# Optimization experiments

Hardware: AMD Instinct MI355X
Metric: run time of the kernel (lower is better)

## Reference

```python
import jax, jax.numpy as jnp
import numpy as np

NQ = 9  # 9 qubits per 3x3 patch; state shape (M, 2,...,2), axis (NQ-q) holds qubit q (qiskit little-endian)

def _ax(q):
    return NQ - q

def _bcast(theta):
    theta = jnp.asarray(theta)
    if theta.ndim == 1:  # per-patch angle -> broadcast over 8 remaining qubit axes
        return theta.reshape((-1,) + (1,) * (NQ - 1))
    return theta

def apply_1q(state, q, m00, m01, m10, m11):
    ax = _ax(q)
    s0 = jnp.take(state, 0, axis=ax)
    s1 = jnp.take(state, 1, axis=ax)
    return jnp.stack([m00 * s0 + m01 * s1, m10 * s0 + m11 * s1], axis=ax)

def apply_ry(state, q, theta):
    th = _bcast(theta) * 0.5
    c = jnp.cos(th).astype(state.dtype)
    s = jnp.sin(th).astype(state.dtype)
    return apply_1q(state, q, c, -s, s, c)

def apply_rz(state, q, theta):
    th = _bcast(theta) * 0.5
    e = jnp.exp(-1j * th.astype(jnp.complex64))
    return apply_1q(state, q, e, 0.0, 0.0, jnp.conj(e))

def apply_cx(state, c, t):
    axc, axt = _ax(c), _ax(t)
    sc0 = jnp.take(state, 0, axis=axc)
    sc1 = jnp.take(state, 1, axis=axc)
    axt2 = axt - 1 if axt > axc else axt
    sc1 = jnp.flip(sc1, axis=axt2)  # X on target within control=1 subspace
    return jnp.stack([sc0, sc1], axis=axc)

def apply_crx(state, c, t, theta):
    axc, axt = _ax(c), _ax(t)
    sc0 = jnp.take(state, 0, axis=axc)
    sc1 = jnp.take(state, 1, axis=axc)
    axt2 = axt - 1 if axt > axc else axt
    t0 = jnp.take(sc1, 0, axis=axt2)
    t1 = jnp.take(sc1, 1, axis=axt2)
    co = jnp.cos(theta * 0.5)
    si = jnp.sin(theta * 0.5)
    sc1 = jnp.stack([co * t0 - 1j * si * t1, -1j * si * t0 + co * t1], axis=axt2)
    return jnp.stack([sc0, sc1], axis=axc)

def qcnn_batched(angles, w):
    """angles: (M, 9) input rotation angles. w: (42,) shared weights. Returns (M, 3) = [<X>,<Y>,<Z>] on qubit 0."""
    M = angles.shape[0]
    state = jnp.zeros((M,) + (2,) * NQ, dtype=jnp.complex64)
    state = state.at[(slice(None),) + (0,) * NQ].set(1.0)
    for q in range(NQ):  # input encoding
        state = apply_ry(state, q, angles[:, q])
    wi = 0
    # conv1: RY + RZ on all 9 qubits, ring CNOT
    for q in range(NQ):
        state = apply_ry(state, q, w[wi]); wi += 1
    for q in range(NQ):
        state = apply_rz(state, q, w[wi]); wi += 1
    for i in range(NQ):
        state = apply_cx(state, i, (i + 1) % NQ)
    # pool1: 6 CRX gates
    for (c, t) in [(1, 0), (2, 0), (4, 3), (5, 3), (7, 6), (8, 6)]:
        state = apply_crx(state, c, t, w[wi]); wi += 1
    # conv2 on qubits [0,3,6]
    for q in [0, 3, 6]:
        state = apply_ry(state, q, w[wi]); wi += 1
    for q in [0, 3, 6]:
        state = apply_rz(state, q, w[wi]); wi += 1
    for (c, t) in [(0, 3), (3, 6), (6, 0)]:
        state = apply_cx(state, c, t)
    state = apply_ry(state, 0, w[wi])
    state = apply_rz(state, 3, w[wi + 1]); wi += 2
    # pool2
    state = apply_crx(state, 3, 0, w[wi])
    state = apply_crx(state, 3, 6, w[wi + 1])
    state = apply_ry(state, 0, w[wi + 2])
    state = apply_ry(state, 6, w[wi + 3]); wi += 4
    # conv3
    state = apply_ry(state, 0, w[wi])
    state = apply_ry(state, 6, w[wi + 1])
    state = apply_cx(state, 0, 6)
    state = apply_rz(state, 0, w[wi + 2])
    state = apply_rz(state, 6, w[wi + 3]); wi += 4
    # pool3
    state = apply_crx(state, 6, 0, w[wi])
    state = apply_ry(state, 0, w[wi + 1]); wi += 2
    assert wi == 42
    # expectations <X>,<Y>,<Z> on qubit 0 (last axis)
    a0 = jnp.take(state, 0, axis=NQ)
    a1 = jnp.take(state, 1, axis=NQ)
    axes = tuple(range(1, NQ))
    z = jnp.sum(jnp.conj(a0) * a1, axis=axes)
    ex = 2.0 * jnp.real(z)
    ey = 2.0 * jnp.imag(z)
    ez = jnp.sum(jnp.abs(a0) ** 2 - jnp.abs(a1) ** 2, axis=axes)
    return jnp.stack([ex, ey, ez], axis=-1).astype(jnp.float32)

def setup_inputs() -> dict:
    key = jax.random.key(0)
    k1, k2, k3 = jax.random.split(key, 3)
    B, H, WS, NCLS = 8, 28, 3, 10
    n = H - WS + 1  # 26 patches per side
    x = jax.random.uniform(k1, (B, 1, H, H), dtype=jnp.float32)
    w = jax.random.normal(k2, (42,), dtype=jnp.float32)
    fc_w = jax.random.normal(k3, (NCLS, n * n * 3), dtype=jnp.float32) * 0.02
    fc_b = jnp.zeros((NCLS,), dtype=jnp.float32)
    return {"x": x, "w": w, "fc_w": fc_w, "fc_b": fc_b}

def reference(x, w, fc_w, fc_b):
    B, H, WS = x.shape[0], x.shape[2], 3
    n = H - WS + 1
    # extract 3x3 patches, row-major within window (matches torch unfold+view)
    patches = jnp.stack([x[:, 0, i:i + n, j:j + n] for i in range(WS) for j in range(WS)], axis=-1)  # (B,n,n,9)
    angles = patches.reshape(B * n * n, WS * WS) * jnp.pi
    bloch = qcnn_batched(angles, w)  # (B*N, 3)
    feats = bloch.reshape(B, n * n * 3)  # patch-major [X,Y,Z] per patch, matches torch.cat over patches
    return feats @ fc_w.T + fc_b
```

## Files before the change

kernel.cpp:

```cpp
#include <hip/hip_runtime.h>


__device__ __forceinline__ float shx(float v, int m) { return __shfl_xor(v, m, 64); }

__device__ __forceinline__ float2 cmul(float2 a, float2 b) {
  return make_float2(a.x * b.x - a.y * b.y, a.x * b.y + a.y * b.x);
}

template <int TM> __device__ __forceinline__
void ry_r(float (&re)[8], float (&im)[8], float c, float s) {
#pragma unroll
  for (int r0 = 0; r0 < 8; ++r0) if (!(r0 & TM)) {
    const int r1 = r0 | TM;
    float a = re[r0], bb = re[r1];
    re[r0] = c * a - s * bb; re[r1] = s * a + c * bb;
    a = im[r0]; bb = im[r1];
    im[r0] = c * a - s * bb; im[r1] = s * a + c * bb;
  }
}
template <int TM> __device__ __forceinline__
void rz_r(float (&re)[8], float (&im)[8], float c, float s) {
#pragma unroll
  for (int r = 0; r < 8; ++r) {
    const float sg = (r & TM) ? s : -s;
    const float a = re[r], bb = im[r];
    re[r] = c * a - sg * bb;
    im[r] = c * bb + sg * a;
  }
}
template <int CM, int TM> __device__ __forceinline__
void cx_rr(float (&re)[8], float (&im)[8]) {
#pragma unroll
  for (int r0 = 0; r0 < 8; ++r0) if ((r0 & CM) && !(r0 & TM)) {
    const int r1 = r0 | TM;
    float t = re[r0]; re[r0] = re[r1]; re[r1] = t;
    t = im[r0]; im[r0] = im[r1]; im[r1] = t;
  }
}
template <int CM, int TM> __device__ __forceinline__
void crx_rr(float (&re)[8], float (&im)[8], float co, float si) {
#pragma unroll
  for (int r0 = 0; r0 < 8; ++r0) if ((r0 & CM) && !(r0 & TM)) {
    const int r1 = r0 | TM;
    const float r0r = re[r0], r0i = im[r0], r1r = re[r1], r1i = im[r1];
    re[r0] = co * r0r + si * r1i; im[r0] = co * r0i - si * r1r;
    re[r1] = co * r1r + si * r0i; im[r1] = co * r1i - si * r0r;
  }
}

__device__ __forceinline__
void ry_f(float2& A, float2& B, float c, float s) {
  const float2 nA = make_float2(c * A.x - s * B.x, c * A.y - s * B.y);
  const float2 nB = make_float2(s * A.x + c * B.x, s * A.y + c * B.y);
  A = nA; B = nB;
}
__device__ __forceinline__
void rz_f(float2& A, float2& B, float c, float s) {
  A = make_float2(c * A.x + s * A.y, c * A.y - s * A.x);
  B = make_float2(c * B.x - s * B.y, c * B.y + s * B.x);
}
__device__ __forceinline__
void rx_f(float2& A, float2& B, float c, float s) {
  const float2 nA = make_float2(c * A.x + s * B.y, c * A.y - s * B.x);
  const float2 nB = make_float2(c * B.x + s * A.y, c * B.y - s * A.x);
  A = nA; B = nB;
}

__global__ __launch_bounds__(256) void qcnn_fused(const float* __restrict__ x,
                                                  const float* __restrict__ w,
                                                  float* __restrict__ feats) {
  __shared__ float4 tauT[4][9];
  __shared__ float2 rxT[4][12];
  __shared__ float2 gT[4][16];

  const int tid = threadIdx.x;
  const int wv = tid >> 6, lane = tid & 63;
  const unsigned p = blockIdx.x * 4u + wv;
  const unsigned b = p / 676u;
  const unsigned rem = p - b * 676u;
  const unsigned i = rem / 26u, j = rem - i * 26u;

  if (lane < 9) {
    const int di = lane / 3, dj = lane - di * 3;
    const float xv = x[b * 784u + (i + di) * 28u + (j + dj)];
    const float ang = fmaf(xv, 3.14159265358979323846f, w[lane]) * 0.5f;
    float s, c; __sincosf(ang, &s, &c);
    float zs, zc; __sincosf(0.5f * w[9 + lane], &zs, &zc);
    tauT[wv][lane] = make_float4(c * zc, -c * zs, s * zc, s * zs);
  } else if (lane < 21) {
    const int k = lane - 9, a = k >> 2, cb = k & 3;
    float th = 0.0f;
    if (cb & 1) th += w[18 + 2 * a];
    if (cb & 2) th += w[19 + 2 * a];
    float s, c; __sincosf(0.5f * th, &s, &c);
    rxT[wv][k] = make_float2(c, s);
  } else if (lane < 37) {
    const int k = lane - 21;
    float th;
    if (k < 10)       th = w[24 + k];
    else if (k == 10) th = w[34] + w[36];
    else if (k == 11) th = w[35] + w[37];
    else              th = w[26 + k];
    float s, c; __sincosf(0.5f * th, &s, &c);
    gT[wv][k] = make_float2(c, s);
  }

  const int l0 = lane & 1, l1 = (lane >> 1) & 1, l2 = (lane >> 2) & 1;
  const int l3 = (lane >> 3) & 1, l4 = (lane >> 4) & 1, l5 = (lane >> 5) & 1;

  float4 tq[9];
#pragma unroll
  for (int q = 0; q < 9; ++q) tq[q] = tauT[wv][q];
  auto tau = [&](int bit, int q) -> float2 {
    const float4 t = tq[q];
    return bit ? make_float2(t.z, t.w) : make_float2(t.x, t.y);
  };

  const int a0 = l5, a1 = l0 ^ l5;
  float2 p00 = cmul(tau(a0, 0), tau(a1, 1));
  float2 p01 = cmul(tau(a0 ^ 1, 0), tau(a1 ^ 1, 1));
  float2 p10 = cmul(tau(l1, 3), tau(l2, 4));
  float2 p11 = cmul(tau(l1 ^ 1, 3), tau(l2 ^ 1, 4));
  float2 p20 = cmul(tau(l3, 6), tau(l4, 7));
  float2 p21 = cmul(tau(l3 ^ 1, 6), tau(l4 ^ 1, 7));
  const float2 T = cmul(cmul(tau(l0 ^ l1, 2), tau(l2 ^ l3, 5)), tau(l4 ^ l5, 8));
  p20 = cmul(p20, T);
  p21 = cmul(p21, T);

  {
    const float2 x0 = rxT[wv][lane & 3];
    const float2 x1 = rxT[wv][4 + ((lane >> 2) & 3)];
    const float2 x2 = rxT[wv][8 + ((lane >> 4) & 3)];
    rx_f(p00, p01, x0.x, x0.y);
    rx_f(p10, p11, x1.x, x1.y);
    rx_f(p20, p21, x2.x, x2.y);
  }

  {
    const float2 g0 = gT[wv][0], g1 = gT[wv][1], g2 = gT[wv][2];
    const float2 g3 = gT[wv][3], g4 = gT[wv][4], g5 = gT[wv][5];
    ry_f(p00, p01, g0.x, g0.y);
    ry_f(p10, p11, g1.x, g1.y);
    ry_f(p20, p21, g2.x, g2.y);
    rz_f(p00, p01, g3.x, g3.y);
    rz_f(p10, p11, g4.x, g4.y);
    rz_f(p20, p21, g5.x, g5.y);
  }

  float re[8], im[8];
  {
    const float2 q00 = cmul(p00, p10);
    const float2 q01 = cmul(p00, p11);
    const float2 q10 = cmul(p01, p10);
    const float2 q11 = cmul(p01, p11);
    float2 u;
    u = cmul(q00, p20); re[0] = u.x; im[0] = u.y;
    u = cmul(q11, p20); re[1] = u.x; im[1] = u.y;
    u = cmul(q01, p21); re[2] = u.x; im[2] = u.y;
    u = cmul(q10, p21); re[3] = u.x; im[3] = u.y;
    u = cmul(q11, p21); re[4] = u.x; im[4] = u.y;
    u = cmul(q00, p21); re[5] = u.x; im[5] = u.y;
    u = cmul(q10, p20); re[6] = u.x; im[6] = u.y;
    u = cmul(q01, p20); re[7] = u.x; im[7] = u.y;
  }

  {
    const float2 g6 = gT[wv][6],  g8 = gT[wv][8];
    const float2 g9 = gT[wv][9],  gA = gT[wv][10], gB = gT[wv][11];
    const float2 gC = gT[wv][12], gE = gT[wv][14];
    ry_r<1>(re, im, g6.x, g6.y);
    crx_rr<2, 1>(re, im, g8.x, g8.y);
    crx_rr<2, 4>(re, im, g9.x, g9.y);
    ry_r<1>(re, im, gA.x, gA.y);
    ry_r<4>(re, im, gB.x, gB.y);
    cx_rr<1, 4>(re, im);
    rz_r<1>(re, im, gC.x, gC.y);
    crx_rr<4, 1>(re, im, gE.x, gE.y);
  }

  float zr = 0.f, zi = 0.f, pe = 0.f;
#pragma unroll
  for (int r0 = 0; r0 < 8; r0 += 2) {
    const int r1 = r0 + 1;
    zr += re[r0] * re[r1] + im[r0] * im[r1];
    zi += re[r0] * im[r1] - im[r0] * re[r1];
    pe += re[r0] * re[r0] + im[r0] * im[r0];
  }
#pragma unroll
  for (int m = 1; m < 64; m <<= 1) { zr += shx(zr, m); zi += shx(zi, m); pe += shx(pe, m); }

  if (lane == 0) {
    const float2 gF = gT[wv][15];
    const float cT = gF.x * gF.x - gF.y * gF.y;
    const float sT = 2.0f * gF.x * gF.y;
    const float ex = 2.0f * zr;
    const float ez = 2.0f * pe - 1.0f;
    feats[p * 3u + 0u] = cT * ex + sT * ez;
    feats[p * 3u + 1u] = 2.0f * zi;
    feats[p * 3u + 2u] = cT * ez - sT * ex;
  }
}

__global__ __launch_bounds__(256) void fc_kernel(const float* __restrict__ feats,
                                                 const float* __restrict__ fc_w,
                                                 const float* __restrict__ fc_b,
                                                 float* __restrict__ out) {
  const int b = blockIdx.x / 10, c = blockIdx.x - b * 10;
  const float4* f  = reinterpret_cast<const float4*>(feats + b * 2028);
  const float4* wr = reinterpret_cast<const float4*>(fc_w + c * 2028);
  float acc = 0.0f;
  for (int k = threadIdx.x; k < 507; k += 256) {
    const float4 fv = f[k], wv4 = wr[k];
    acc += fv.x * wv4.x + fv.y * wv4.y + fv.z * wv4.z + fv.w * wv4.w;
  }
#pragma unroll
  for (int m = 1; m < 64; m <<= 1) acc += __shfl_xor(acc, m, 64);
  __shared__ float sbuf[4];
  const int lane = threadIdx.x & 63, wv = threadIdx.x >> 6;
  if (lane == 0) sbuf[wv] = acc;
  __syncthreads();
  if (threadIdx.x == 0) out[b * 10 + c] = sbuf[0] + sbuf[1] + sbuf[2] + sbuf[3] + fc_b[c];
}

extern "C" void kernel_launch(void* const* d_in, const int* in_sizes, int n_in,
                              void* d_out, int out_size, void* d_ws, size_t ws_size,
                              hipStream_t stream) {
  const float* x    = (const float*)d_in[0];
  const float* w    = (const float*)d_in[1];
  const float* fc_w = (const float*)d_in[2];
  const float* fc_b = (const float*)d_in[3];
  float* out = (float*)d_out;

  const int B = in_sizes[0] / 784;
  const int npatch = B * 676;

  float* feats = (float*)d_ws;

  qcnn_fused<<<npatch / 4, 256, 0, stream>>>(x, w, feats);
  fc_kernel<<<B * 10, 256, 0, stream>>>(feats, fc_w, fc_b, out);
}
```

Baseline: 67.19 us.

## Fuse consecutive single-qubit gates into precomputed 2x2 complex matrices

Merges the RX/RY/RZ gate sequences on the per-lane factors into one 2x2 complex matrix per lane group. It also rewrites the register-level gate chain into fused pair-wise 2x2 matrix applications with re-derived commuted angles. The matrices are computed once per block by wave 0 and shared through LDS. This adds a __syncthreads and more per-block setup on one wave, in exchange for fewer FLOPs per lane. Correctness depends on the hand-derived gate commutations.

```diff
diff --git a/kernel.cpp b/kernel.cpp
--- a/kernel.cpp
+++ b/kernel.cpp
@@ -7,26 +7,29 @@
   return make_float2(a.x * b.x - a.y * b.y, a.x * b.y + a.y * b.x);
 }
 
-template <int TM> __device__ __forceinline__
-void ry_r(float (&re)[8], float (&im)[8], float c, float s) {
-#pragma unroll
-  for (int r0 = 0; r0 < 8; ++r0) if (!(r0 & TM)) {
-    const int r1 = r0 | TM;
-    float a = re[r0], bb = re[r1];
-    re[r0] = c * a - s * bb; re[r1] = s * a + c * bb;
-    a = im[r0]; bb = im[r1];
-    im[r0] = c * a - s * bb; im[r1] = s * a + c * bb;
-  }
-}
-template <int TM> __device__ __forceinline__
-void rz_r(float (&re)[8], float (&im)[8], float c, float s) {
-#pragma unroll
-  for (int r = 0; r < 8; ++r) {
-    const float sg = (r & TM) ? s : -s;
-    const float a = re[r], bb = im[r];
-    re[r] = c * a - sg * bb;
-    im[r] = c * bb + sg * a;
-  }
+__device__ __forceinline__
+void g2_f(float2& A, float2& B, float4 R0, float4 R1) {
+  const float2 nA = make_float2(R0.x*A.x - R0.y*A.y + R0.z*B.x - R0.w*B.y,
+                                R0.x*A.y + R0.y*A.x + R0.z*B.y + R0.w*B.x);
+  const float2 nB = make_float2(R1.x*A.x - R1.y*A.y + R1.z*B.x - R1.w*B.y,
+                                R1.x*A.y + R1.y*A.x + R1.z*B.y + R1.w*B.x);
+  A = nA; B = nB;
+}
+
+template <int RA, int RB> __device__ __forceinline__
+void g2_r(float (&re)[8], float (&im)[8], float4 R0, float4 R1) {
+  const float ar = re[RA], ai = im[RA], br = re[RB], bi = im[RB];
+  re[RA] = R0.x*ar - R0.y*ai + R0.z*br - R0.w*bi;
+  im[RA] = R0.x*ai + R0.y*ar + R0.z*bi + R0.w*br;
+  re[RB] = R1.x*ar - R1.y*ai + R1.z*br - R1.w*bi;
+  im[RB] = R1.x*ai + R1.y*ar + R1.z*bi + R1.w*br;
+}
+template <int RA, int RB> __device__ __forceinline__
+void ry_pair(float (&re)[8], float (&im)[8], float c, float s) {
+  float a = re[RA], bb = re[RB];
+  re[RA] = c*a - s*bb; re[RB] = s*a + c*bb;
+  a = im[RA]; bb = im[RB];
+  im[RA] = c*a - s*bb; im[RB] = s*a + c*bb;
 }
 template <int CM, int TM> __device__ __forceinline__
 void cx_rr(float (&re)[8], float (&im)[8]) {
@@ -48,30 +51,12 @@
   }
 }
 
-__device__ __forceinline__
-void ry_f(float2& A, float2& B, float c, float s) {
-  const float2 nA = make_float2(c * A.x - s * B.x, c * A.y - s * B.y);
-  const float2 nB = make_float2(s * A.x + c * B.x, s * A.y + c * B.y);
-  A = nA; B = nB;
-}
-__device__ __forceinline__
-void rz_f(float2& A, float2& B, float c, float s) {
-  A = make_float2(c * A.x + s * A.y, c * A.y - s * A.x);
-  B = make_float2(c * B.x - s * B.y, c * B.y + s * B.x);
-}
-__device__ __forceinline__
-void rx_f(float2& A, float2& B, float c, float s) {
-  const float2 nA = make_float2(c * A.x + s * B.y, c * A.y - s * B.x);
-  const float2 nB = make_float2(c * B.x + s * A.y, c * B.y - s * A.x);
-  A = nA; B = nB;
-}
-
 __global__ __launch_bounds__(256) void qcnn_fused(const float* __restrict__ x,
                                                   const float* __restrict__ w,
                                                   float* __restrict__ feats) {
   __shared__ float4 tauT[4][9];
-  __shared__ float2 rxT[4][12];
-  __shared__ float2 gT[4][16];
+  __shared__ float4 matT[30];
+  __shared__ float2 sT[3];
 
   const int tid = threadIdx.x;
   const int wv = tid >> 6, lane = tid & 63;
@@ -87,23 +72,51 @@
     float s, c; __sincosf(ang, &s, &c);
     float zs, zc; __sincosf(0.5f * w[9 + lane], &zs, &zc);
     tauT[wv][lane] = make_float4(c * zc, -c * zs, s * zc, s * zs);
-  } else if (lane < 21) {
-    const int k = lane - 9, a = k >> 2, cb = k & 3;
-    float th = 0.0f;
-    if (cb & 1) th += w[18 + 2 * a];
-    if (cb & 2) th += w[19 + 2 * a];
-    float s, c; __sincosf(0.5f * th, &s, &c);
-    rxT[wv][k] = make_float2(c, s);
-  } else if (lane < 37) {
-    const int k = lane - 21;
-    float th;
-    if (k < 10)       th = w[24 + k];
-    else if (k == 10) th = w[34] + w[36];
-    else if (k == 11) th = w[35] + w[37];
-    else              th = w[26 + k];
-    float s, c; __sincosf(0.5f * th, &s, &c);
-    gT[wv][k] = make_float2(c, s);
-  }
+  }
+
+  if (wv == 0) {
+    const bool isF = (lane >= 9 && lane < 21);
+    const bool isM = (lane >= 24 && lane < 27);
+    if (isF || isM) {
+      float a = 0.f, bb = 0.f, c = 0.f, z = 0.f;
+      int dst;
+      if (isF) {
+        const int k = lane - 9, ax = k >> 2, cb2 = k & 3;
+        bb = ((cb2 & 1) ? w[18 + 2 * ax] : 0.f) + ((cb2 & 2) ? w[19 + 2 * ax] : 0.f);
+        c = w[24 + ax]; z = w[27 + ax];
+        dst = k;
+      } else {
+        const int m = lane - 24;
+        if (m == 0)      { a = w[30] + w[34] + w[36]; z = w[38]; }
+        else if (m == 1) { a = w[30]; bb = w[32]; c = w[34] + w[36]; z = w[38]; }
+        else             { bb = w[33]; c = w[35] + w[37]; }
+        dst = 12 + m;
+      }
+      float sa, ca, sb, cb, sc, cc, sz, cz;
+      __sincosf(0.5f * a,  &sa, &ca);
+      __sincosf(0.5f * bb, &sb, &cb);
+      __sincosf(0.5f * c,  &sc, &cc);
+      __sincosf(0.5f * z,  &sz, &cz);
+      const float A00r =  cb * ca, A00i = -sb * sa;
+      const float A01r = -cb * sa, A01i = -sb * ca;
+      const float A10r =  cb * sa, A10i = -sb * ca;
+      const float A11r =  cb * ca, A11i =  sb * sa;
+      const float B00r = cc * A00r - sc * A10r, B00i = cc * A00i - sc * A10i;
+      const float B01r = cc * A01r - sc * A11r, B01i = cc * A01i - sc * A11i;
+      const float B10r = sc * A00r + cc * A10r, B10i = sc * A00i + cc * A10i;
+      const float B11r = sc * A01r + cc * A11r, B11i = sc * A01i + cc * A11i;
+      matT[dst * 2 + 0] = make_float4(cz * B00r + sz * B00i, cz * B00i - sz * B00r,
+                                      cz * B01r + sz * B01i, cz * B01i - sz * B01r);
+      matT[dst * 2 + 1] = make_float4(cz * B10r - sz * B10i, cz * B10i + sz * B10r,
+                                      cz * B11r - sz * B11i, cz * B11i + sz * B11r);
+    } else if (lane >= 27 && lane < 30) {
+      const int k = lane - 27;
+      const float th = (k == 0) ? w[40] : (k == 1) ? w[41] : (w[35] + w[37]);
+      float s, c; __sincosf(0.5f * th, &s, &c);
+      sT[k] = make_float2(c, s);
+    }
+  }
+  __syncthreads();
 
   const int l0 = lane & 1, l1 = (lane >> 1) & 1, l2 = (lane >> 2) & 1;
   const int l3 = (lane >> 3) & 1, l4 = (lane >> 4) & 1, l5 = (lane >> 5) & 1;
@@ -128,23 +141,12 @@
   p21 = cmul(p21, T);
 
   {
-    const float2 x0 = rxT[wv][lane & 3];
-    const float2 x1 = rxT[wv][4 + ((lane >> 2) & 3)];
-    const float2 x2 = rxT[wv][8 + ((lane >> 4) & 3)];
-    rx_f(p00, p01, x0.x, x0.y);
-    rx_f(p10, p11, x1.x, x1.y);
-    rx_f(p20, p21, x2.x, x2.y);
-  }
-
-  {
-    const float2 g0 = gT[wv][0], g1 = gT[wv][1], g2 = gT[wv][2];
-    const float2 g3 = gT[wv][3], g4 = gT[wv][4], g5 = gT[wv][5];
-    ry_f(p00, p01, g0.x, g0.y);
-    ry_f(p10, p11, g1.x, g1.y);
-    ry_f(p20, p21, g2.x, g2.y);
-    rz_f(p00, p01, g3.x, g3.y);
-    rz_f(p10, p11, g4.x, g4.y);
-    rz_f(p20, p21, g5.x, g5.y);
+    const int i0 = (lane & 3) << 1;
+    const int i1 = (4 + ((lane >> 2) & 3)) << 1;
+    const int i2 = (8 + ((lane >> 4) & 3)) << 1;
+    g2_f(p00, p01, matT[i0], matT[i0 | 1]);
+    g2_f(p10, p11, matT[i1], matT[i1 | 1]);
+    g2_f(p20, p21, matT[i2], matT[i2 | 1]);
   }
 
   float re[8], im[8];
@@ -165,17 +167,17 @@
   }
 
   {
-    const float2 g6 = gT[wv][6],  g8 = gT[wv][8];
-    const float2 g9 = gT[wv][9],  gA = gT[wv][10], gB = gT[wv][11];
-    const float2 gC = gT[wv][12], gE = gT[wv][14];
-    ry_r<1>(re, im, g6.x, g6.y);
-    crx_rr<2, 1>(re, im, g8.x, g8.y);
-    crx_rr<2, 4>(re, im, g9.x, g9.y);
-    ry_r<1>(re, im, gA.x, gA.y);
-    ry_r<4>(re, im, gB.x, gB.y);
+    const float4 A0 = matT[24], A1 = matT[25];
+    const float4 B0 = matT[26], B1 = matT[27];
+    const float4 C0 = matT[28], C1 = matT[29];
+    const float2 s2 = sT[2];
+    g2_r<0, 1>(re, im, A0, A1); g2_r<4, 5>(re, im, A0, A1);
+    g2_r<2, 3>(re, im, B0, B1); g2_r<6, 7>(re, im, B0, B1);
+    ry_pair<0, 4>(re, im, s2.x, s2.y); ry_pair<1, 5>(re, im, s2.x, s2.y);
+    g2_r<2, 6>(re, im, C0, C1); g2_r<3, 7>(re, im, C0, C1);
     cx_rr<1, 4>(re, im);
-    rz_r<1>(re, im, gC.x, gC.y);
-    crx_rr<4, 1>(re, im, gE.x, gE.y);
+    const float2 sE = sT[0];
+    crx_rr<4, 1>(re, im, sE.x, sE.y);
   }
 
   float zr = 0.f, zi = 0.f, pe = 0.f;
@@ -190,14 +192,14 @@
   for (int m = 1; m < 64; m <<= 1) { zr += shx(zr, m); zi += shx(zi, m); pe += shx(pe, m); }
 
   if (lane == 0) {
-    const float2 gF = gT[wv][15];
+    const float2 gF = sT[1];
     const float cT = gF.x * gF.x - gF.y * gF.y;
-    const float sT = 2.0f * gF.x * gF.y;
+    const float sTT = 2.0f * gF.x * gF.y;
     const float ex = 2.0f * zr;
     const float ez = 2.0f * pe - 1.0f;
-    feats[p * 3u + 0u] = cT * ex + sT * ez;
+    feats[p * 3u + 0u] = cT * ex + sTT * ez;
     feats[p * 3u + 1u] = 2.0f * zi;
-    feats[p * 3u + 2u] = cT * ez - sT * ex;
+    feats[p * 3u + 2u] = cT * ez - sTT * ex;
   }
 }
 
```

Result: faster. 65.84 us (-2.0%).
